# Kernel tuning notes

Measured on AMD Instinct MI355X. Metric: run time of the kernel, lower is better.

The kernel has to match this reference:

```python
import jax, jax.numpy as jnp
import numpy as np

B, T_E, T_D, H = 32, 128, 128, 256  # batch, encoder len, decoder len, hidden


def lstm_scan(x, h0, c0, Wih, Whh, bih, bhh):
    """Single-layer PyTorch-style LSTM over x: [B, T, F] -> (hs, cs) each [T, B, H]."""
    bias = bih + bhh

    def step(carry, xt):
        h, c = carry
        gates = xt @ Wih.T + h @ Whh.T + bias  # [B, 4H], gate order i,f,g,o
        i, f, g, o = jnp.split(gates, 4, axis=-1)
        i = jax.nn.sigmoid(i)
        f = jax.nn.sigmoid(f)
        o = jax.nn.sigmoid(o)
        g = jnp.tanh(g)
        c = f * c + i * g
        h = o * jnp.tanh(c)
        return (h, c), (h, c)

    _, (hs, cs) = jax.lax.scan(step, (h0, c0), jnp.swapaxes(x, 0, 1))
    return hs, cs


def setup_inputs() -> dict:
    key = jax.random.key(0)
    ks = jax.random.split(key, 16)
    seq = jax.random.normal(ks[0], (B, T_E), jnp.float32)
    seq_m = jax.random.randint(ks[1], (B, 1), 1, T_E + 1)  # valid lengths in [1, T_E]
    pos = jnp.arange(T_E)[None, :]
    seq = jnp.where(pos < seq_m, seq, 0.0)  # zero-pad beyond length (drives the mask)
    target = jax.random.normal(ks[2], (B, T_D), jnp.float32)

    s = 0.1
    nrm = lambda k, shape: s * jax.random.normal(k, shape, jnp.float32)
    return dict(
        seq=seq, seq_m=seq_m, target=target,
        Wih_e=nrm(ks[3], (4 * H, 1)), Whh_e=nrm(ks[4], (4 * H, H)),
        bih_e=nrm(ks[5], (4 * H,)), bhh_e=nrm(ks[6], (4 * H,)),
        Wih_d=nrm(ks[7], (4 * H, 1)), Whh_d=nrm(ks[8], (4 * H, H)),
        bih_d=nrm(ks[9], (4 * H,)), bhh_d=nrm(ks[10], (4 * H,)),
        We=nrm(ks[11], (H, H)), be=nrm(ks[12], (H,)),
        Wd=nrm(ks[13], (H, H)), bd=nrm(ks[14], (H,)),
        v=jnp.ones((H,), jnp.float32),
    )


def reference(seq, seq_m, target,
              Wih_e, Whh_e, bih_e, bhh_e,
              Wih_d, Whh_d, bih_d, bhh_d,
              We, be, Wd, bd, v):
    zeros = jnp.zeros((B, H), seq.dtype)
    # Encoder: one fused scan instead of the original per-timestep Python loop
    hs_e, cs_e = lstm_scan(seq[..., None], zeros, zeros, Wih_e, Whh_e, bih_e, bhh_e)
    e = jnp.swapaxes(hs_e, 0, 1)  # [B, T_E, H]

    # Grab encoder state at the last valid step (seq_m - 1) per batch element
    last = seq_m[:, 0] - 1  # [B]
    bidx = jnp.arange(B)
    e_hs = hs_e[last, bidx]  # [B, H]
    e_cs = cs_e[last, bidx]

    # Decoder initialized from the selected encoder state
    hs_d, _ = lstm_scan(target[..., None], e_hs, e_cs, Wih_d, Whh_d, bih_d, bhh_d)
    d = jnp.swapaxes(hs_d, 0, 1)  # [B, T_D, H]

    e2 = e @ We.T + be  # [B, T_E, H]
    d2 = d @ Wd.T + bd  # [B, T_D, H]

    # Additive (Bahdanau) attention: tanh(e_j + d_i) . v  -> [B, T_D, T_E]
    t = jnp.tanh(d2[:, :, None, :] + e2[:, None, :, :])  # [B, T_D, T_E, H]
    p = jnp.einsum('bijh,h->bij', t, v)

    # Masking: original sets seq[:,0]=0.1 then adds 1000 where seq value nonzero,
    # after subtracting 1000 everywhere -> padded (zero) positions end up at -1000.
    seq0 = seq.at[:, 0].set(0.1)
    mask = (seq0 != 0).astype(p.dtype)  # [B, T_E]
    p = p + (mask[:, None, :] - 1.0) * 1000.0

    return jax.nn.softmax(p, axis=-1)  # pointer distribution over encoder positions
```

## Files before the change

kernel.cpp:

```cpp
#include <hip/hip_runtime.h>
#include <hip/hip_bf16.h>

#define BB 32
#define TT 128
#define HH 256
#define G4 4
#define UPB 64
#define RPB 256

#define AGENT __HIP_MEMORY_SCOPE_AGENT
#define AL(p) __hip_atomic_load((p), __ATOMIC_RELAXED, AGENT)

__device__ __forceinline__ float rcp_f(float x) { return __builtin_amdgcn_rcpf(x); }
__device__ __forceinline__ float sigmoid_f(float x) {
    return rcp_f(1.f + __expf(-x));
}
__device__ __forceinline__ float tanh_f(float x) {
    float e = __expf(2.f * x);
    return 1.f - 2.f * rcp_f(e + 1.f);
}

__global__ __launch_bounds__(512, 2) void lstm_kernel(
    const float* __restrict__ seq,
    const int* __restrict__ seq_m,
    const float* __restrict__ target,
    const float* __restrict__ Wih_e,
    const float* __restrict__ Whh_e,
    const float* __restrict__ bih_e, const float* __restrict__ bhh_e,
    const float* __restrict__ Wih_d, const float* __restrict__ Whh_d,
    const float* __restrict__ bih_d, const float* __restrict__ bhh_d,
    const float* __restrict__ We, const float* __restrict__ be,
    const float* __restrict__ Wd, const float* __restrict__ bd,
    float* __restrict__ e2,
    float* __restrict__ d2,
    unsigned long long* __restrict__ mbox,
    unsigned long long* __restrict__ hsave)
{
    const int blk = blockIdx.x;
    const int b = blk & 31;
    const int g = blk >> 5;
    const int tid = threadIdx.x;
    const int row_local = tid >> 1;
    const int half = tid & 1;
    const int gate = row_local >> 6;
    const int u_local = row_local & 63;
    const int row_global = gate * HH + g * UPB + u_local;
    const int last = seq_m[b] - 1;
    const int s = tid - 256;
    const int pu = s >> 2;
    const int kq = s & 3;
    const int pcol = g * UPB + pu;

    __shared__ float hbuf[2][HH];
    __shared__ float g_lds[RPB];
    __shared__ float x_lds[2 * TT];
    __shared__ float h_final[HH];

    for (int i = tid; i < TT; i += 512) {
        x_lds[i] = seq[b * TT + i];
        x_lds[TT + i] = target[b * TT + i];
    }

    float4 w[32];
    float bias_r, wih_r;
    auto loadw = [&](const float* Whh, const float* Wih,
                     const float* bih, const float* bhh) {
        const float4* wr = (const float4*)(Whh + row_global * HH + half * 128);
#pragma unroll
        for (int i = 0; i < 32; ++i) w[i] = wr[i];
        bias_r = bih[row_global] + bhh[row_global];
        wih_r = Wih[row_global];
    };
    loadw(Whh_e, Wih_e, bih_e, bhh_e);

    float4 pw[16];
    float pb = 0.f;
    auto loadp = [&](const float* W, const float* bias) {
        const float4* src = (const float4*)(W + pcol * HH + kq * 64);
#pragma unroll
        for (int i = 0; i < 16; ++i) pw[i] = src[i];
        pb = bias[pcol];
    };
    if (tid >= 256) loadp(We, be);

    auto projdot = [&](const float* hsrc) -> float {
        const float4* hp = (const float4*)(hsrc + kq * 64);
        float pa = 0.f;
#pragma unroll
        for (int i = 0; i < 16; ++i) {
            float4 hv = hp[i];
            pa = fmaf(pw[i].x, hv.x, pa);
            pa = fmaf(pw[i].y, hv.y, pa);
            pa = fmaf(pw[i].z, hv.z, pa);
            pa = fmaf(pw[i].w, hv.w, pa);
        }
        pa += __shfl_xor(pa, 1);
        pa += __shfl_xor(pa, 2);
        return pa + pb;
    };

    if (tid < 64) {
        ((float4*)hbuf[1])[tid] = make_float4(0.f, 0.f, 0.f, 0.f);
    }
    __syncthreads();

    float c = 0.f, c_saved = 0.f, h_saved = 0.f;

    for (int t = 0; t < 2 * TT; ++t) {
        const int phase = t >> 7;
        const int tt = t & 127;
        const float x = x_lds[t];
        const int rb = (t & 1) ^ 1;

        const float4* h4 = ((const float4*)hbuf[rb]) + half * 32;
        float4 a4 = make_float4(0.f, 0.f, 0.f, 0.f);
#pragma unroll
        for (int i = 0; i < 32; ++i) {
            float4 hv = h4[i];
            a4.x = fmaf(w[i].x, hv.x, a4.x);
            a4.y = fmaf(w[i].y, hv.y, a4.y);
            a4.z = fmaf(w[i].z, hv.z, a4.z);
            a4.w = fmaf(w[i].w, hv.w, a4.w);
        }
        float acc = (a4.x + a4.y) + (a4.z + a4.w);
        acc += __shfl_xor(acc, 1);
        float gv = acc + bias_r + x * wih_r;
        if (half == 0) g_lds[row_local] = gv;
        __syncthreads();

        if (tid < 64) {
            float gi = g_lds[tid];
            float gf = g_lds[64 + tid];
            float gg = g_lds[128 + tid];
            float go = g_lds[192 + tid];
            float si = sigmoid_f(gi);
            float sf = sigmoid_f(gf);
            float tg = tanh_f(gg);
            float so = sigmoid_f(go);
            c = sf * c + si * tg;
            float h = so * tanh_f(c);
            const int ug = g * UPB + tid;
            unsigned long long pkt =
                ((unsigned long long)(unsigned)(t + 1) << 32) | __float_as_uint(h);
            __hip_atomic_store(&mbox[(t & 1) * BB * HH + b * HH + ug], pkt,
                               __ATOMIC_RELAXED, AGENT);
            if (phase == 0 && tt == last) {
                c_saved = c;
                h_saved = h;
                unsigned long long spkt =
                    (1ull << 32) | (unsigned long long)__float_as_uint(h);
                __hip_atomic_store(&hsave[b * HH + ug], spkt, __ATOMIC_RELAXED, AGENT);
            }
            hbuf[t & 1][ug] = (t == TT - 1) ? h_saved : h;
        }

        if (tid >= 64 && tid < 256) {
            const int p = (g + (tid >> 6)) & 3;
            const int lane = tid & 63;
            const int ppu = p * UPB + lane;
            unsigned long long* src;
            unsigned want;
            if (t == TT - 1) {
                src = &hsave[b * HH + ppu];
                want = 1u;
            } else {
                src = &mbox[(t & 1) * BB * HH + b * HH + ppu];
                want = (unsigned)(t + 1);
            }
            unsigned long long pv;
            {
                unsigned long long r0 = AL(src);
                unsigned long long r1 = AL(src);
                unsigned long long r2 = AL(src);
                unsigned long long r3 = AL(src);
                for (;;) {
                    if ((unsigned)(r0 >> 32) == want) { pv = r0; break; }
                    r0 = AL(src);
                    if ((unsigned)(r1 >> 32) == want) { pv = r1; break; }
                    r1 = AL(src);
                    if ((unsigned)(r2 >> 32) == want) { pv = r2; break; }
                    r2 = AL(src);
                    if ((unsigned)(r3 >> 32) == want) { pv = r3; break; }
                    r3 = AL(src);
                }
            }
            hbuf[t & 1][ppu] = __uint_as_float((unsigned)pv);
        }

        if (tid >= 256 && t >= 1) {
            const float* hsrc = (t == TT) ? h_final : hbuf[rb];
            float pv = projdot(hsrc);
            if (kq == 0) {
                if (t <= TT)
                    e2[(b * TT + (t - 1)) * HH + pcol] = pv;
                else
                    d2[(b * TT + (t - 1 - TT)) * HH + pcol] = pv;
            }
        }
        if (tid >= 256 && t == TT - 1) {
            unsigned long long* src = &mbox[((TT - 1) & 1) * BB * HH + b * HH + s];
            const unsigned want = (unsigned)TT;
            unsigned long long r0 = AL(src);
            unsigned long long r1 = AL(src);
            unsigned long long pv;
            for (;;) {
                if ((unsigned)(r0 >> 32) == want) { pv = r0; break; }
                r0 = AL(src);
                if ((unsigned)(r1 >> 32) == want) { pv = r1; break; }
                r1 = AL(src);
            }
            h_final[s] = __uint_as_float((unsigned)pv);
        }
        if (tid >= 256 && t == TT) loadp(Wd, bd);

        __syncthreads();

        if (t == TT - 1) {
            loadw(Whh_d, Wih_d, bih_d, bhh_d);
            c = c_saved;
        }
    }

    if (tid >= 256) {
        unsigned long long* src = &mbox[((2 * TT - 1) & 1) * BB * HH + b * HH + s];
        const unsigned want = (unsigned)(2 * TT);
        unsigned long long r0 = AL(src);
        unsigned long long r1 = AL(src);
        unsigned long long pv;
        for (;;) {
            if ((unsigned)(r0 >> 32) == want) { pv = r0; break; }
            r0 = AL(src);
            if ((unsigned)(r1 >> 32) == want) { pv = r1; break; }
            r1 = AL(src);
        }
        h_final[s] = __uint_as_float((unsigned)pv);
    }
    __syncthreads();
    if (tid >= 256) {
        float pv = projdot(h_final);
        if (kq == 0) d2[(b * TT + (TT - 1)) * HH + pcol] = pv;
    }
}

#define EPAD 260
__global__ __launch_bounds__(256) void attn_p_kernel(
    const float* __restrict__ e2, const float* __restrict__ d2,
    const float* __restrict__ vv, float* __restrict__ p_ws) {
    __shared__ float e2c[32][EPAD];
    __shared__ float d2t[32][EPAD];
    __shared__ float v_lds[HH];

    const int blk = blockIdx.x;
    const int b = blk >> 4;
    const int i0 = ((blk >> 2) & 3) * 32;
    const int j0 = (blk & 3) * 32;
    const int tid = threadIdx.x;
    const int jl = tid & 31, ig = tid >> 5;

    if (tid < 64) *(float4*)&v_lds[tid * 4] = ((const float4*)vv)[tid];
    for (int idx = tid; idx < 32 * 64; idx += 256) {
        int r = idx >> 6, q = idx & 63;
        *(float4*)&d2t[r][q * 4] = ((const float4*)(d2 + (b * TT + i0 + r) * HH))[q];
        *(float4*)&e2c[r][q * 4] = ((const float4*)(e2 + (b * TT + j0 + r) * HH))[q];
    }
    __syncthreads();

    float a0 = 0.f, a1 = 0.f, a2 = 0.f, a3 = 0.f;
    for (int h = 0; h < HH; h += 4) {
        float4 ev = *(const float4*)&e2c[jl][h];
        float4 vx = *(const float4*)&v_lds[h];
        float4 d0 = *(const float4*)&d2t[ig * 4 + 0][h];
        float4 d1 = *(const float4*)&d2t[ig * 4 + 1][h];
        float4 d2v = *(const float4*)&d2t[ig * 4 + 2][h];
        float4 d3 = *(const float4*)&d2t[ig * 4 + 3][h];
        a0 = fmaf(tanh_f(ev.x + d0.x), vx.x, a0);
        a0 = fmaf(tanh_f(ev.y + d0.y), vx.y, a0);
        a0 = fmaf(tanh_f(ev.z + d0.z), vx.z, a0);
        a0 = fmaf(tanh_f(ev.w + d0.w), vx.w, a0);
        a1 = fmaf(tanh_f(ev.x + d1.x), vx.x, a1);
        a1 = fmaf(tanh_f(ev.y + d1.y), vx.y, a1);
        a1 = fmaf(tanh_f(ev.z + d1.z), vx.z, a1);
        a1 = fmaf(tanh_f(ev.w + d1.w), vx.w, a1);
        a2 = fmaf(tanh_f(ev.x + d2v.x), vx.x, a2);
        a2 = fmaf(tanh_f(ev.y + d2v.y), vx.y, a2);
        a2 = fmaf(tanh_f(ev.z + d2v.z), vx.z, a2);
        a2 = fmaf(tanh_f(ev.w + d2v.w), vx.w, a2);
        a3 = fmaf(tanh_f(ev.x + d3.x), vx.x, a3);
        a3 = fmaf(tanh_f(ev.y + d3.y), vx.y, a3);
        a3 = fmaf(tanh_f(ev.z + d3.z), vx.z, a3);
        a3 = fmaf(tanh_f(ev.w + d3.w), vx.w, a3);
    }
    float* pr = p_ws + (b * TT + i0 + ig * 4) * TT + j0 + jl;
    pr[0 * TT] = a0;
    pr[1 * TT] = a1;
    pr[2 * TT] = a2;
    pr[3 * TT] = a3;
}

__global__ __launch_bounds__(256) void attn_sm_kernel(
    const float* __restrict__ p_ws, const float* __restrict__ seq,
    float* __restrict__ out) {
    const int blk = blockIdx.x;
    const int b = blk >> 3;
    const int r0 = (blk & 7) * 16;
    const int tid = threadIdx.x;
    const int r = tid >> 4, l16 = tid & 15;
    const int row = (b * TT + r0 + r) * TT;

    float xr[8];
    float m = -1e30f;
#pragma unroll
    for (int k = 0; k < 8; ++k) {
        const int j = l16 + 16 * k;
        float x = p_ws[row + j];
        float sv = (j == 0) ? 0.1f : seq[b * TT + j];
        if (sv == 0.f) x -= 1000.f;
        xr[k] = x;
        m = fmaxf(m, x);
    }
#pragma unroll
    for (int o = 8; o >= 1; o >>= 1) m = fmaxf(m, __shfl_xor(m, o));
    float s = 0.f;
#pragma unroll
    for (int k = 0; k < 8; ++k) {
        xr[k] = __expf(xr[k] - m);
        s += xr[k];
    }
#pragma unroll
    for (int o = 8; o >= 1; o >>= 1) s += __shfl_xor(s, o);
    float inv = rcp_f(s);
#pragma unroll
    for (int k = 0; k < 8; ++k) out[row + l16 + 16 * k] = xr[k] * inv;
}

extern "C" void kernel_launch(void* const* d_in, const int* in_sizes, int n_in,
                              void* d_out, int out_size, void* d_ws, size_t ws_size,
                              hipStream_t stream) {
    const float* seq = (const float*)d_in[0];
    const int* seq_m = (const int*)d_in[1];
    const float* target = (const float*)d_in[2];
    const float* Wih_e = (const float*)d_in[3];
    const float* Whh_e = (const float*)d_in[4];
    const float* bih_e = (const float*)d_in[5];
    const float* bhh_e = (const float*)d_in[6];
    const float* Wih_d = (const float*)d_in[7];
    const float* Whh_d = (const float*)d_in[8];
    const float* bih_d = (const float*)d_in[9];
    const float* bhh_d = (const float*)d_in[10];
    const float* We = (const float*)d_in[11];
    const float* be = (const float*)d_in[12];
    const float* Wd = (const float*)d_in[13];
    const float* bd = (const float*)d_in[14];
    const float* vv = (const float*)d_in[15];

    float* ws = (float*)d_ws;
    const size_t SZ_ED = (size_t)BB * TT * HH;
    float* e2 = ws;
    float* d2 = e2 + SZ_ED;
    float* p_ws = d2 + SZ_ED;
    unsigned long long* mbox =
        (unsigned long long*)(p_ws + (size_t)BB * TT * TT);
    unsigned long long* hsave = mbox + 2 * BB * HH;

    const size_t needed = (2 * SZ_ED + (size_t)BB * TT * TT) * sizeof(float) +
                          3 * BB * HH * sizeof(unsigned long long);
    if (ws_size < needed) return;

    hipMemsetAsync(mbox, 0, 3 * BB * HH * sizeof(unsigned long long), stream);
    lstm_kernel<<<BB * G4, 512, 0, stream>>>(seq, seq_m, target, Wih_e, Whh_e, bih_e,
                                             bhh_e, Wih_d, Whh_d, bih_d, bhh_d, We,
                                             be, Wd, bd, e2, d2, mbox, hsave);
    attn_p_kernel<<<512, 256, 0, stream>>>(e2, d2, vv, p_ws);
    attn_sm_kernel<<<256, 256, 0, stream>>>(p_ws, seq, (float*)d_out);
}
```

Before: 600.1 us.

## Split LSTM recurrence by input columns and exchange partial gate sums

```diff
diff --git a/kernel.cpp b/kernel.cpp
--- a/kernel.cpp
+++ b/kernel.cpp
@@ -6,10 +6,10 @@
 #define HH 256
 #define G4 4
 #define UPB 64
-#define RPB 256
 
 #define AGENT __HIP_MEMORY_SCOPE_AGENT
 #define AL(p) __hip_atomic_load((p), __ATOMIC_RELAXED, AGENT)
+#define AS(p, v) __hip_atomic_store((p), (v), __ATOMIC_RELAXED, AGENT)
 
 __device__ __forceinline__ float rcp_f(float x) { return __builtin_amdgcn_rcpf(x); }
 __device__ __forceinline__ float sigmoid_f(float x) {
@@ -33,45 +33,63 @@
     const float* __restrict__ Wd, const float* __restrict__ bd,
     float* __restrict__ e2,
     float* __restrict__ d2,
-    unsigned long long* __restrict__ mbox,
-    unsigned long long* __restrict__ hsave)
+    unsigned long long* __restrict__ mbox_p,
+    unsigned long long* __restrict__ mbox_h)
 {
     const int blk = blockIdx.x;
     const int b = blk & 31;
     const int g = blk >> 5;
     const int tid = threadIdx.x;
-    const int row_local = tid >> 1;
-    const int half = tid & 1;
-    const int gate = row_local >> 6;
-    const int u_local = row_local & 63;
-    const int row_global = gate * HH + g * UPB + u_local;
     const int last = seq_m[b] - 1;
+
+    const int r0 = tid << 1;
+    const int gate_t = r0 >> 8;
+    const int unit0 = r0 & 255;
+    const int owner = unit0 >> 6;
+    const int uo = (gate_t << 6) | (unit0 & 63);
+    const int slot_s = (g - owner + 3) & 3;
+
+    const int q = tid - 64;
+    const int pslot = q >> 6;
+    const int plane = q & 63;
+
     const int s = tid - 256;
     const int pu = s >> 2;
     const int kq = s & 3;
     const int pcol = g * UPB + pu;
 
-    __shared__ float hbuf[2][HH];
-    __shared__ float g_lds[RPB];
+    __shared__ float h_lds[UPB];
+    __shared__ float own_p[256];
+    __shared__ float psum[3 * 256];
     __shared__ float x_lds[2 * TT];
-    __shared__ float h_final[HH];
+    __shared__ float h_full[2][HH];
 
     for (int i = tid; i < TT; i += 512) {
         x_lds[i] = seq[b * TT + i];
         x_lds[TT + i] = target[b * TT + i];
     }
 
-    float4 w[32];
-    float bias_r, wih_r;
-    auto loadw = [&](const float* Whh, const float* Wih,
-                     const float* bih, const float* bhh) {
-        const float4* wr = (const float4*)(Whh + row_global * HH + half * 128);
-#pragma unroll
-        for (int i = 0; i < 32; ++i) w[i] = wr[i];
-        bias_r = bih[row_global] + bhh[row_global];
-        wih_r = Wih[row_global];
+    float4 w0[16], w1[16];
+    auto loadw = [&](const float* Whh) {
+        const float4* a = (const float4*)(Whh + r0 * HH + g * UPB);
+        const float4* c2 = (const float4*)(Whh + (r0 + 1) * HH + g * UPB);
+#pragma unroll
+        for (int i = 0; i < 16; ++i) { w0[i] = a[i]; w1[i] = c2[i]; }
     };
-    loadw(Whh_e, Wih_e, bih_e, bhh_e);
+    loadw(Whh_e);
+
+    float bact[4], wact[4];
+    auto loadact = [&](const float* Wih, const float* bih, const float* bhh) {
+        if (tid < 64) {
+#pragma unroll
+            for (int k = 0; k < 4; ++k) {
+                const int rg = k * HH + g * UPB + tid;
+                bact[k] = bih[rg] + bhh[rg];
+                wact[k] = Wih[rg];
+            }
+        }
+    };
+    loadact(Wih_e, bih_e, bhh_e);
 
     float4 pw[16];
     float pb = 0.f;
@@ -99,9 +117,7 @@
         return pa + pb;
     };
 
-    if (tid < 64) {
-        ((float4*)hbuf[1])[tid] = make_float4(0.f, 0.f, 0.f, 0.f);
-    }
+    if (tid < 64) h_lds[tid] = 0.f;
     __syncthreads();
 
     float c = 0.f, c_saved = 0.f, h_saved = 0.f;
@@ -109,30 +125,94 @@
     for (int t = 0; t < 2 * TT; ++t) {
         const int phase = t >> 7;
         const int tt = t & 127;
-        const float x = x_lds[t];
-        const int rb = (t & 1) ^ 1;
-
-        const float4* h4 = ((const float4*)hbuf[rb]) + half * 32;
-        float4 a4 = make_float4(0.f, 0.f, 0.f, 0.f);
-#pragma unroll
-        for (int i = 0; i < 32; ++i) {
-            float4 hv = h4[i];
-            a4.x = fmaf(w[i].x, hv.x, a4.x);
-            a4.y = fmaf(w[i].y, hv.y, a4.y);
-            a4.z = fmaf(w[i].z, hv.z, a4.z);
-            a4.w = fmaf(w[i].w, hv.w, a4.w);
-        }
-        float acc = (a4.x + a4.y) + (a4.z + a4.w);
-        acc += __shfl_xor(acc, 1);
-        float gv = acc + bias_r + x * wih_r;
-        if (half == 0) g_lds[row_local] = gv;
+        const int par = t & 1;
+        const unsigned tag = (unsigned)(t + 1);
+
+        float a0 = 0.f, a1 = 0.f;
+        const float4* hp = (const float4*)h_lds;
+#pragma unroll
+        for (int i = 0; i < 16; ++i) {
+            float4 hv = hp[i];
+            a0 = fmaf(w0[i].x, hv.x, a0);
+            a0 = fmaf(w0[i].y, hv.y, a0);
+            a0 = fmaf(w0[i].z, hv.z, a0);
+            a0 = fmaf(w0[i].w, hv.w, a0);
+            a1 = fmaf(w1[i].x, hv.x, a1);
+            a1 = fmaf(w1[i].y, hv.y, a1);
+            a1 = fmaf(w1[i].z, hv.z, a1);
+            a1 = fmaf(w1[i].w, hv.w, a1);
+        }
+        if (owner == g) {
+            *(float2*)&own_p[uo] = make_float2(a0, a1);
+        } else {
+            unsigned long long* dst =
+                mbox_p + ((size_t)(par * BB + b) * 3 + slot_s) * 1024 + r0;
+            AS(dst, ((unsigned long long)tag << 32) | __float_as_uint(a0));
+            AS(dst + 1, ((unsigned long long)tag << 32) | __float_as_uint(a1));
+        }
+
+        if (tid >= 64 && tid < 256) {
+            unsigned long long* base =
+                mbox_p + ((size_t)(par * BB + b) * 3 + pslot) * 1024 + g * UPB + plane;
+            unsigned long long* p0 = base;
+            unsigned long long* p1 = base + 256;
+            unsigned long long* p2 = base + 512;
+            unsigned long long* p3 = base + 768;
+            unsigned long long c0 = AL(p0), c1 = AL(p1), c2v = AL(p2), c3 = AL(p3);
+            for (;;) {
+                const bool e0 = (unsigned)(c0 >> 32) == tag;
+                const bool e1 = (unsigned)(c1 >> 32) == tag;
+                const bool e2v = (unsigned)(c2v >> 32) == tag;
+                const bool e3 = (unsigned)(c3 >> 32) == tag;
+                if (e0 & e1 & e2v & e3) break;
+                if (!e0) c0 = AL(p0);
+                if (!e1) c1 = AL(p1);
+                if (!e2v) c2v = AL(p2);
+                if (!e3) c3 = AL(p3);
+            }
+            psum[pslot * 256 + 0 + plane] = __uint_as_float((unsigned)c0);
+            psum[pslot * 256 + 64 + plane] = __uint_as_float((unsigned)c1);
+            psum[pslot * 256 + 128 + plane] = __uint_as_float((unsigned)c2v);
+            psum[pslot * 256 + 192 + plane] = __uint_as_float((unsigned)c3);
+        }
+
+        if (tid >= 256) {
+            if (t >= 1) {
+                unsigned long long* hsrc =
+                    mbox_h + (size_t)(((t - 1) & 1) * BB + b) * HH + s;
+                unsigned long long r = AL(hsrc);
+                while ((unsigned)(r >> 32) != (unsigned)t) r = AL(hsrc);
+                h_full[(t - 1) & 1][s] = __uint_as_float((unsigned)r);
+            }
+            if (t >= 2) {
+                const int row = t - 2;
+                float pv = projdot(h_full[par]);
+                if (kq == 0) {
+                    if (row < TT)
+                        e2[(b * TT + row) * HH + pcol] = pv;
+                    else
+                        d2[(b * TT + row - TT) * HH + pcol] = pv;
+                }
+                if (t == TT + 1) loadp(Wd, bd);
+            }
+        }
+
         __syncthreads();
 
         if (tid < 64) {
-            float gi = g_lds[tid];
-            float gf = g_lds[64 + tid];
-            float gg = g_lds[128 + tid];
-            float go = g_lds[192 + tid];
+            const float x = x_lds[t];
+            float gi = own_p[0 * 64 + tid] + psum[0 * 256 + 0 * 64 + tid] +
+                       psum[1 * 256 + 0 * 64 + tid] + psum[2 * 256 + 0 * 64 + tid] +
+                       bact[0] + x * wact[0];
+            float gf = own_p[1 * 64 + tid] + psum[0 * 256 + 1 * 64 + tid] +
+                       psum[1 * 256 + 1 * 64 + tid] + psum[2 * 256 + 1 * 64 + tid] +
+                       bact[1] + x * wact[1];
+            float gg = own_p[2 * 64 + tid] + psum[0 * 256 + 2 * 64 + tid] +
+                       psum[1 * 256 + 2 * 64 + tid] + psum[2 * 256 + 2 * 64 + tid] +
+                       bact[2] + x * wact[2];
+            float go = own_p[3 * 64 + tid] + psum[0 * 256 + 3 * 64 + tid] +
+                       psum[1 * 256 + 3 * 64 + tid] + psum[2 * 256 + 3 * 64 + tid] +
+                       bact[3] + x * wact[3];
             float si = sigmoid_f(gi);
             float sf = sigmoid_f(gf);
             float tg = tanh_f(gg);
@@ -140,105 +220,36 @@
             c = sf * c + si * tg;
             float h = so * tanh_f(c);
             const int ug = g * UPB + tid;
-            unsigned long long pkt =
-                ((unsigned long long)(unsigned)(t + 1) << 32) | __float_as_uint(h);
-            __hip_atomic_store(&mbox[(t & 1) * BB * HH + b * HH + ug], pkt,
-                               __ATOMIC_RELAXED, AGENT);
+            AS(&mbox_h[(size_t)(par * BB + b) * HH + ug],
+               ((unsigned long long)tag << 32) | __float_as_uint(h));
             if (phase == 0 && tt == last) {
                 c_saved = c;
                 h_saved = h;
-                unsigned long long spkt =
-                    (1ull << 32) | (unsigned long long)__float_as_uint(h);
-                __hip_atomic_store(&hsave[b * HH + ug], spkt, __ATOMIC_RELAXED, AGENT);
-            }
-            hbuf[t & 1][ug] = (t == TT - 1) ? h_saved : h;
-        }
-
-        if (tid >= 64 && tid < 256) {
-            const int p = (g + (tid >> 6)) & 3;
-            const int lane = tid & 63;
-            const int ppu = p * UPB + lane;
-            unsigned long long* src;
-            unsigned want;
-            if (t == TT - 1) {
-                src = &hsave[b * HH + ppu];
-                want = 1u;
-            } else {
-                src = &mbox[(t & 1) * BB * HH + b * HH + ppu];
-                want = (unsigned)(t + 1);
-            }
-            unsigned long long pv;
-            {
-                unsigned long long r0 = AL(src);
-                unsigned long long r1 = AL(src);
-                unsigned long long r2 = AL(src);
-                unsigned long long r3 = AL(src);
-                for (;;) {
-                    if ((unsigned)(r0 >> 32) == want) { pv = r0; break; }
-                    r0 = AL(src);
-                    if ((unsigned)(r1 >> 32) == want) { pv = r1; break; }
-                    r1 = AL(src);
-                    if ((unsigned)(r2 >> 32) == want) { pv = r2; break; }
-                    r2 = AL(src);
-                    if ((unsigned)(r3 >> 32) == want) { pv = r3; break; }
-                    r3 = AL(src);
-                }
-            }
-            hbuf[t & 1][ppu] = __uint_as_float((unsigned)pv);
-        }
-
-        if (tid >= 256 && t >= 1) {
-            const float* hsrc = (t == TT) ? h_final : hbuf[rb];
-            float pv = projdot(hsrc);
-            if (kq == 0) {
-                if (t <= TT)
-                    e2[(b * TT + (t - 1)) * HH + pcol] = pv;
-                else
-                    d2[(b * TT + (t - 1 - TT)) * HH + pcol] = pv;
-            }
-        }
-        if (tid >= 256 && t == TT - 1) {
-            unsigned long long* src = &mbox[((TT - 1) & 1) * BB * HH + b * HH + s];
-            const unsigned want = (unsigned)TT;
-            unsigned long long r0 = AL(src);
-            unsigned long long r1 = AL(src);
-            unsigned long long pv;
-            for (;;) {
-                if ((unsigned)(r0 >> 32) == want) { pv = r0; break; }
-                r0 = AL(src);
-                if ((unsigned)(r1 >> 32) == want) { pv = r1; break; }
-                r1 = AL(src);
-            }
-            h_final[s] = __uint_as_float((unsigned)pv);
-        }
-        if (tid >= 256 && t == TT) loadp(Wd, bd);
+            }
+            h_lds[tid] = (t == TT - 1) ? h_saved : h;
+        }
 
         __syncthreads();
 
         if (t == TT - 1) {
-            loadw(Whh_d, Wih_d, bih_d, bhh_d);
+            loadw(Whh_d);
+            loadact(Wih_d, bih_d, bhh_d);
             c = c_saved;
         }
     }
 
     if (tid >= 256) {
-        unsigned long long* src = &mbox[((2 * TT - 1) & 1) * BB * HH + b * HH + s];
-        const unsigned want = (unsigned)(2 * TT);
-        unsigned long long r0 = AL(src);
-        unsigned long long r1 = AL(src);
-        unsigned long long pv;
-        for (;;) {
-            if ((unsigned)(r0 >> 32) == want) { pv = r0; break; }
-            r0 = AL(src);
-            if ((unsigned)(r1 >> 32) == want) { pv = r1; break; }
-            r1 = AL(src);
-        }
-        h_final[s] = __uint_as_float((unsigned)pv);
+        float pv = projdot(h_full[0]);
+        if (kq == 0) d2[(b * TT + TT - 2) * HH + pcol] = pv;
+        unsigned long long* hsrc = mbox_h + (size_t)(1 * BB + b) * HH + s;
+        unsigned long long r = AL(hsrc);
+        while ((unsigned)(r >> 32) != (unsigned)(2 * TT)) r = AL(hsrc);
+        h_full[1][s] = __uint_as_float((unsigned)r);
     }
     __syncthreads();
     if (tid >= 256) {
-        float pv = projdot(h_final);
-        if (kq == 0) d2[(b * TT + (TT - 1)) * HH + pcol] = pv;
+        float pv = projdot(h_full[1]);
+        if (kq == 0) d2[(b * TT + TT - 1) * HH + pcol] = pv;
     }
 }
 
@@ -358,18 +369,19 @@
     float* e2 = ws;
     float* d2 = e2 + SZ_ED;
     float* p_ws = d2 + SZ_ED;
-    unsigned long long* mbox =
+    unsigned long long* mbox_p =
         (unsigned long long*)(p_ws + (size_t)BB * TT * TT);
-    unsigned long long* hsave = mbox + 2 * BB * HH;
-
+    unsigned long long* mbox_h = mbox_p + (size_t)2 * BB * 3 * 1024;
+
+    const size_t n_pkts = (size_t)2 * BB * 3 * 1024 + (size_t)2 * BB * HH;
     const size_t needed = (2 * SZ_ED + (size_t)BB * TT * TT) * sizeof(float) +
-                          3 * BB * HH * sizeof(unsigned long long);
+                          n_pkts * sizeof(unsigned long long);
     if (ws_size < needed) return;
 
-    hipMemsetAsync(mbox, 0, 3 * BB * HH * sizeof(unsigned long long), stream);
+    hipMemsetAsync(mbox_p, 0, n_pkts * sizeof(unsigned long long), stream);
     lstm_kernel<<<BB * G4, 512, 0, stream>>>(seq, seq_m, target, Wih_e, Whh_e, bih_e,
                                              bhh_e, Wih_d, Whh_d, bih_d, bhh_d, We,
-                                             be, Wd, bd, e2, d2, mbox, hsave);
+                                             be, Wd, bd, e2, d2, mbox_p, mbox_h);
     attn_p_kernel<<<512, 256, 0, stream>>>(e2, d2, vv, p_ws);
     attn_sm_kernel<<<256, 256, 0, stream>>>(p_ws, seq, (float*)d_out);
 }
```

Result: slower. 769.3 us (+28.2%).
